# Performance work log

Measured on AMD Instinct MI355X. Metric: run time of the kernel, lower is better.

## Reference

```python
import jax, jax.numpy as jnp
import numpy as np
import math

N, E = 20000, 200000
MUL = 128            # multiplicity of the 0e and 1o channels
D = MUL + 3 * MUL    # 512 = node feature dim
EDGE_ATTR = 32
HID = 32             # invariant_neurons
LOG2 = math.log(2.0)


def ssp(x):
    # ShiftedSoftPlus
    return jax.nn.softplus(x) - LOG2


def split_irreps(x):
    # x: [?, 512] -> (l=0 part [?, MUL], l=1 part [?, MUL, 3])
    return x[:, :MUL], x[:, MUL:].reshape(x.shape[0], MUL, 3)


def merge_irreps(x0, x1):
    return jnp.concatenate([x0, x1.reshape(x1.shape[0], MUL * 3)], axis=-1)


def irrep_linear(x, W0, b0, W1):
    # e3nn o3.Linear: per-irrep channel mixing; bias only on l=0
    x0, x1 = split_irreps(x)
    y0 = x0 @ W0 + b0
    y1 = jnp.einsum('nuc,uv->nvc', x1, W1)
    return merge_irreps(y0, y1)


def setup_inputs() -> dict:
    key = jax.random.key(0)
    ks = iter(jax.random.split(key, 32))

    def randn(shape, scale=1.0):
        return (scale * jax.random.normal(next(ks), shape)).astype(jnp.float32)

    inp = {
        'x': randn((N, D)),
        'edge_sh': randn((E, 4)),
        'edge_attr': jax.random.uniform(next(ks), (E, EDGE_ATTR), dtype=jnp.float32),
        'edge_index': jax.random.randint(next(ks), (2, E), 0, N, dtype=jnp.int32),
        # linear_node_pre
        'W_pre0': randn((MUL, MUL), MUL ** -0.5), 'b_pre0': jnp.zeros((MUL,), jnp.float32),
        'W_pre1': randn((MUL, MUL), MUL ** -0.5),
        # linear_node
        'W_nd0': randn((MUL, MUL), MUL ** -0.5), 'b_nd0': jnp.zeros((MUL,), jnp.float32),
        'W_nd1': randn((MUL, MUL), MUL ** -0.5),
        # NormGate fc: Linear(2*MUL,2*MUL)+SiLU+Linear(2*MUL,2*MUL)
        'W_g1': randn((2 * MUL, 2 * MUL), (2 * MUL) ** -0.5), 'b_g1': jnp.zeros((2 * MUL,), jnp.float32),
        'W_g2': randn((2 * MUL, 2 * MUL), (2 * MUL) ** -0.5), 'b_g2': jnp.zeros((2 * MUL,), jnp.float32),
        # fc_node: FullyConnectedNet([32, 32, 4*MUL], ssp) -- no biases
        'W_f1': randn((EDGE_ATTR, HID), EDGE_ATTR ** -0.5),
        'W_f2': randn((HID, 4 * MUL), HID ** -0.5),
        # layer_l0: FullyConnectedNet([3*MUL, 32, 4*MUL], ssp)
        'W_s1': randn((3 * MUL, HID), (3 * MUL) ** -0.5),
        'W_s2': randn((HID, 4 * MUL), HID ** -0.5),
        # linear_out
        'W_o0': randn((MUL, MUL), MUL ** -0.5), 'b_o0': jnp.zeros((MUL,), jnp.float32),
        'W_o1': randn((MUL, MUL), MUL ** -0.5),
    }
    return inp


def reference(x, edge_sh, edge_attr, edge_index,
              W_pre0, b_pre0, W_pre1, W_nd0, b_nd0, W_nd1,
              W_g1, b_g1, W_g2, b_g2, W_f1, W_f2, W_s1, W_s2,
              W_o0, b_o0, W_o1):
    edge_dst, edge_src = edge_index[0], edge_index[1]
    old_x = x

    # ---- s0 edge invariants: linear_node_pre + InnerProduct (uuu, /dim)
    pre = irrep_linear(x, W_pre0, b_pre0, W_pre1)
    p0, p1 = split_irreps(pre)
    pd0 = p0[edge_dst]
    ip1 = jnp.einsum('eum,eum->eu', p1[edge_dst], p1[edge_src]) / 3.0   # l=1 inner product [E, MUL]
    s0 = jnp.concatenate([pd0, pd0, ip1], axis=-1)                      # [E, 3*MUL]

    # ---- NormGate then linear_node on node features
    x0, x1 = split_irreps(x)
    n1 = jnp.sqrt(jnp.sum(x1 * x1, axis=-1) / 3.0)                      # per-irrep norm [N, MUL]
    g = jax.nn.silu(jnp.concatenate([x0, n1], -1) @ W_g1 + b_g1) @ W_g2 + b_g2
    xg = merge_irreps(g[:, :MUL], x1 * g[:, MUL:, None])
    x = irrep_linear(xg, W_nd0, b_nd0, W_nd1)
    self_x = x

    # ---- per-edge tensor-product weights (fc_node(edge_attr) * layer_l0(s0))
    w = (ssp(edge_attr @ W_f1) @ W_f2) * (ssp(s0 @ W_s1) @ W_s2)        # [E, 4*MUL]
    w1, w2, w3, w4 = jnp.split(w, 4, axis=-1)

    # ---- gather + equivariant tensor product with edge spherical harmonics (uvu paths)
    x0e, x1e = split_irreps(x[edge_src])
    sh0, sh1 = edge_sh[:, 0], edge_sh[:, 1:4]
    # paths: 0e*0e->0e, 1o*1o->0e (dot), 0e*1o->1o, 1o*0e->1o
    out0 = w1 * x0e * sh0[:, None] + w4 * (jnp.einsum('eum,em->eu', x1e, sh1) / jnp.sqrt(3.0))
    out1 = (w2[:, :, None] * x0e[:, :, None] * sh1[:, None, :]
            + w3[:, :, None] * x1e * sh0[:, None, None])
    edge_feat = merge_irreps(out0, out1)                                # [E, D]

    # ---- scatter messages back to destination nodes
    out = jax.ops.segment_sum(edge_feat, edge_dst, num_segments=old_x.shape[0])
    out = out + self_x                                                  # irrep_in == irrep_out skip
    out = irrep_linear(out, W_o0, b_o0, W_o1)
    return out + old_x                                                  # ConvNetLayer resnet
```

## Files before the change

### kernel.cpp

```cpp
#include <hip/hip_runtime.h>
#include <hip/hip_fp16.h>
#include <math.h>

#define NN 20000
#define EE 200000

__device__ __forceinline__ float sspf(float x){
    float sp = (x > 20.f) ? x : log1pf(expf(x));
    return sp - 0.69314718056f;
}

__device__ __forceinline__ void fma8(float* acc, const float* base, float w){
    const float4 a = ((const float4*)base)[0];
    const float4 b = ((const float4*)base)[1];
    acc[0]+=a.x*w; acc[1]+=a.y*w; acc[2]+=a.z*w; acc[3]+=a.w*w;
    acc[4]+=b.x*w; acc[5]+=b.y*w; acc[6]+=b.z*w; acc[7]+=b.w*w;
}

__global__ __launch_bounds__(256) void k_pre(
    const float* __restrict__ x, const float* __restrict__ Wp0,
    const float* __restrict__ bp0, const float* __restrict__ Wp1,
    const float* __restrict__ Ws1,
    float* __restrict__ p1, float* __restrict__ sdst)
{
    __shared__ float xl[512][8];
    __shared__ float p0l[8][128];
    const int tid = threadIdx.x;
    const int n0 = blockIdx.x * 8;

    for (int it = 0; it < 4; ++it){
        int idx = tid + 256*it;
        int node = idx >> 7, o4 = idx & 127;
        float4 v = ((const float4*)(x + (size_t)(n0+node)*512))[o4];
        xl[o4*4+0][node]=v.x; xl[o4*4+1][node]=v.y;
        xl[o4*4+2][node]=v.z; xl[o4*4+3][node]=v.w;
    }
    __syncthreads();

    const int j = tid;
    float acc1[8] = {0,0,0,0,0,0,0,0};
    float acc2[8] = {0,0,0,0,0,0,0,0};
    const int o2 = j + 128;
    const int v2 = o2/3, m2 = o2%3;

    if (j < 128){
        for (int u = 0; u < 128; ++u){
            float w1 = Wp0[u*128 + j];
            float w2 = Wp1[u*128 + v2];
            fma8(acc1, &xl[u][0], w1);
            fma8(acc2, &xl[128 + u*3 + m2][0], w2);
        }
        float b = bp0[j];
        #pragma unroll
        for (int n = 0; n < 8; ++n) p0l[n][j] = acc1[n] + b;
    } else {
        const int o1 = j - 128, v1 = o1/3, m1 = o1%3;
        for (int u = 0; u < 128; ++u){
            float w1 = Wp1[u*128 + v1];
            float w2 = Wp1[u*128 + v2];
            fma8(acc1, &xl[128 + u*3 + m1][0], w1);
            fma8(acc2, &xl[128 + u*3 + m2][0], w2);
        }
        #pragma unroll
        for (int n = 0; n < 8; ++n) p1[(size_t)(n0+n)*384 + (j-128)] = acc1[n];
    }
    #pragma unroll
    for (int n = 0; n < 8; ++n) p1[(size_t)(n0+n)*384 + o2] = acc2[n];
    __syncthreads();

    {
        int n = tid >> 5, h = tid & 31;
        float s = 0.f;
        for (int u = 0; u < 128; ++u){
            float wc = Ws1[u*32 + h] + Ws1[(128+u)*32 + h];
            s += p0l[n][u] * wc;
        }
        sdst[(size_t)(n0+n)*32 + h] = s;
    }
}

__global__ __launch_bounds__(256) void k_gate_nd(
    const float* __restrict__ x,
    const float* __restrict__ Wg1, const float* __restrict__ bg1,
    const float* __restrict__ Wg2, const float* __restrict__ bg2,
    const float* __restrict__ Wnd0, const float* __restrict__ bnd0,
    const float* __restrict__ Wnd1,
    float* __restrict__ self_x)
{
    __shared__ float xl[512][8];
    __shared__ float tl[256][8];
    __shared__ float hl[256][8];
    const int tid = threadIdx.x;
    const int n0 = blockIdx.x * 8;

    for (int it = 0; it < 4; ++it){
        int idx = tid + 256*it;
        int node = idx >> 7, o4 = idx & 127;
        float4 v = ((const float4*)(x + (size_t)(n0+node)*512))[o4];
        xl[o4*4+0][node]=v.x; xl[o4*4+1][node]=v.y;
        xl[o4*4+2][node]=v.z; xl[o4*4+3][node]=v.w;
    }
    __syncthreads();

    {
        int jj = tid;
        if (jj < 128){
            #pragma unroll
            for (int n = 0; n < 8; ++n) tl[jj][n] = xl[jj][n];
        } else {
            int u = jj - 128;
            #pragma unroll
            for (int n = 0; n < 8; ++n){
                float a = xl[128+u*3][n], b = xl[128+u*3+1][n], c = xl[128+u*3+2][n];
                tl[jj][n] = sqrtf((a*a + b*b + c*c) * (1.f/3.f));
            }
        }
    }
    __syncthreads();

    {
        float acc[8] = {0,0,0,0,0,0,0,0};
        for (int k = 0; k < 256; ++k){
            float w = Wg1[k*256 + tid];
            fma8(acc, &tl[k][0], w);
        }
        float b = bg1[tid];
        #pragma unroll
        for (int n = 0; n < 8; ++n){
            float v = acc[n] + b;
            hl[tid][n] = v / (1.f + expf(-v));
        }
    }
    __syncthreads();

    {
        float acc[8] = {0,0,0,0,0,0,0,0};
        for (int k = 0; k < 256; ++k){
            float w = Wg2[k*256 + tid];
            fma8(acc, &hl[k][0], w);
        }
        float b = bg2[tid];
        #pragma unroll
        for (int n = 0; n < 8; ++n) tl[tid][n] = acc[n] + b;
    }
    __syncthreads();

    {
        int jj = tid;
        if (jj < 128){
            #pragma unroll
            for (int n = 0; n < 8; ++n) xl[jj][n] = tl[jj][n];
        } else {
            int u = jj - 128;
            #pragma unroll
            for (int n = 0; n < 8; ++n){
                float g1 = tl[128+u][n];
                xl[128+u*3  ][n] *= g1;
                xl[128+u*3+1][n] *= g1;
                xl[128+u*3+2][n] *= g1;
            }
        }
    }
    __syncthreads();

    const int j = tid;
    float acc1[8] = {0,0,0,0,0,0,0,0};
    float acc2[8] = {0,0,0,0,0,0,0,0};
    const int o2 = j + 128;
    const int v2 = o2/3, m2 = o2%3;
    if (j < 128){
        for (int u = 0; u < 128; ++u){
            float w1 = Wnd0[u*128 + j];
            float w2 = Wnd1[u*128 + v2];
            fma8(acc1, &xl[u][0], w1);
            fma8(acc2, &xl[128 + u*3 + m2][0], w2);
        }
        float b = bnd0[j];
        #pragma unroll
        for (int n = 0; n < 8; ++n) self_x[(size_t)(n0+n)*512 + j] = acc1[n] + b;
    } else {
        const int o1 = j - 128, v1 = o1/3, m1 = o1%3;
        for (int u = 0; u < 128; ++u){
            float w1 = Wnd1[u*128 + v1];
            float w2 = Wnd1[u*128 + v2];
            fma8(acc1, &xl[128 + u*3 + m1][0], w1);
            fma8(acc2, &xl[128 + u*3 + m2][0], w2);
        }
        #pragma unroll
        for (int n = 0; n < 8; ++n) self_x[(size_t)(n0+n)*512 + j] = acc1[n];
    }
    #pragma unroll
    for (int n = 0; n < 8; ++n) self_x[(size_t)(n0+n)*512 + j + 256] = acc2[n];
}

__global__ __launch_bounds__(256) void k_count(
    const int* __restrict__ eidx, int* __restrict__ cnt)
{
    int e = blockIdx.x * 256 + threadIdx.x;
    if (e < EE){
        int d = eidx[e];
        if (d >= 0 && d < NN) atomicAdd(&cnt[d], 1);
    }
}

__global__ __launch_bounds__(256) void k_scan(
    const int* __restrict__ cnt, int* __restrict__ rowptr, int* __restrict__ cur)
{
    __shared__ int part[256];
    const int t = threadIdx.x;
    const int CHUNK = 79;
    const int base = t * CHUNK;
    int s = 0;
    for (int i = 0; i < CHUNK; ++i){
        int idx = base + i;
        if (idx < NN) s += cnt[idx];
    }
    part[t] = s;
    __syncthreads();
    for (int off = 1; off < 256; off <<= 1){
        int v = (t >= off) ? part[t-off] : 0;
        __syncthreads();
        part[t] += v;
        __syncthreads();
    }
    int run = (t == 0) ? 0 : part[t-1];
    for (int i = 0; i < CHUNK; ++i){
        int idx = base + i;
        if (idx < NN){
            rowptr[idx] = run;
            cur[idx]    = run;
            run += cnt[idx];
        }
    }
    if (t == 255) rowptr[NN] = run;
}

__global__ __launch_bounds__(256) void k_fill(
    const int* __restrict__ eidx, int* __restrict__ cur, int2* __restrict__ ebuf,
    int* __restrict__ dstbuf)
{
    int e = blockIdx.x * 256 + threadIdx.x;
    if (e < EE){
        int dst = eidx[e];
        int src = eidx[EE + e];
        if (dst >= 0 && dst < NN){
            int pos = atomicAdd(&cur[dst], 1);
            if (pos >= 0 && pos < EE){
                ebuf[pos] = make_int2(e, src);
                dstbuf[pos] = dst;
            }
        }
    }
}

__global__ __launch_bounds__(256, 4) void k_edge_pre(
    const float* __restrict__ p1g, const float* __restrict__ sdst,
    const float* __restrict__ ea,
    const int2* __restrict__ ebuf, const int* __restrict__ dstbuf,
    const float* __restrict__ Wf1, const float* __restrict__ Ws1,
    float* __restrict__ fbuf, float* __restrict__ sbuf)
{
    __shared__ float ipw[4][128];
    const int tid  = threadIdx.x;
    const int wv   = tid >> 6, lane = tid & 63;
    const long e   = (long)blockIdx.x * 4 + wv;

    int2 pe = ebuf[e];
    if (!(pe.x >= 0 && pe.x < EE)) pe.x = 0;
    if (!(pe.y >= 0 && pe.y < NN)) pe.y = 0;
    int dst = dstbuf[e];
    if (!(dst >= 0 && dst < NN)) dst = 0;

    const float* pd = p1g + (size_t)dst*384 + lane*6;
    const float* ps = p1g + (size_t)pe.y*384 + lane*6;
    const float2 d01 = *(const float2*)(pd);
    const float2 d23 = *(const float2*)(pd+2);
    const float2 d45 = *(const float2*)(pd+4);
    const float2 s01 = *(const float2*)(ps);
    const float2 s23 = *(const float2*)(ps+2);
    const float2 s45 = *(const float2*)(ps+4);
    const float ipa = (d01.x*s01.x + d01.y*s01.y + d23.x*s23.x) * (1.f/3.f);
    const float ipb = (d23.y*s23.y + d45.x*s45.x + d45.y*s45.y) * (1.f/3.f);
    *(float2*)&ipw[wv][lane*2] = make_float2(ipa, ipb);

    const int h = lane & 31;
    const float sdv = sdst[(size_t)dst*32 + h];

    __syncthreads();

    const int uh = (lane >> 5) * 64;
    float sA = 0.f, sB = 0.f;
    #pragma unroll 8
    for (int uu = 0; uu < 64; uu += 2){
        sA += ipw[wv][uh+uu]   * Ws1[(256+uh+uu)*32 + h];
        sB += ipw[wv][uh+uu+1] * Ws1[(257+uh+uu)*32 + h];
    }
    float s = sA + sB;
    s += __shfl_xor(s, 32);

    const int kh = (lane >> 5) * 16;
    const float* ear = ea + (size_t)pe.x*32 + kh;
    float f = 0.f;
    #pragma unroll 8
    for (int kk = 0; kk < 16; ++kk)
        f += ear[kk] * Wf1[(kh+kk)*32 + h];
    f += __shfl_xor(f, 32);

    if (lane < 32){
        sbuf[e*32 + h] = sspf(s + sdv);
        fbuf[e*32 + h] = sspf(f);
    }
}

__global__ __launch_bounds__(256) void k_edge_one(
    const float* __restrict__ fbuf, const float* __restrict__ sbuf,
    const float* __restrict__ self_x, const float* __restrict__ esh,
    const int2* __restrict__ ebuf, const int* __restrict__ dstbuf,
    const float* __restrict__ Wf2, const float* __restrict__ Ws2,
    float* __restrict__ out)
{
    __shared__ float fbl[64][32];
    __shared__ float sbl[64][32];
    __shared__ float shl[64][4];
    __shared__ float sxl[4][128];
    __shared__ int   srcl[64], dl[64];

    const int tid = threadIdx.x;
    const int wv  = tid >> 6;
    const int ln  = tid & 63;
    const int c   = tid >> 1;
    const int h   = tid & 1;
    const long e0 = (long)blockIdx.x * 64;
    const float IS3 = 0.57735026919f;

    float wfA[32], wfB[32], wsA[32], wsB[32];
    {
        const int qA = 2*h*128 + c, qB = (2*h+1)*128 + c;
        #pragma unroll
        for (int k = 0; k < 32; ++k){
            wfA[k] = Wf2[(size_t)k*512 + qA];
            wfB[k] = Wf2[(size_t)k*512 + qB];
            wsA[k] = Ws2[(size_t)k*512 + qA];
            wsB[k] = Ws2[(size_t)k*512 + qB];
        }
    }

    if (tid < 64){
        int2 pe = ebuf[e0 + tid];
        if (!(pe.x >= 0 && pe.x < EE)) pe.x = 0;
        if (!(pe.y >= 0 && pe.y < NN)) pe.y = 0;
        int d = dstbuf[e0 + tid];
        if (!(d >= 0 && d < NN)) d = 0;
        srcl[tid] = pe.y; dl[tid] = d;
        ((float4*)shl)[tid] = ((const float4*)esh)[pe.x];
    }
    {
        const float4* fsrc = (const float4*)(fbuf + (size_t)e0*32);
        const float4* ssrc = (const float4*)(sbuf + (size_t)e0*32);
        ((float4*)fbl)[tid]       = fsrc[tid];
        ((float4*)fbl)[tid + 256] = fsrc[tid + 256];
        ((float4*)sbl)[tid]       = ssrc[tid];
        ((float4*)sbl)[tid + 256] = ssrc[tid + 256];
    }
    __syncthreads();

    const int dprev = (blockIdx.x == 0)    ? -1 : dstbuf[e0 - 1];
    const int dnext = (e0 + 64 < EE)       ? dstbuf[e0 + 64] : -1;

    const int goff = (ln < 16) ? (32*wv + 2*ln) : (128 + 96*wv + 2*(ln-16));
    const int loff = (ln < 16) ? (2*ln)         : (32 + 2*(ln-16));
    const int ci   = c & 31;

    float2 rA = *(const float2*)(self_x + (size_t)srcl[0]*512 + goff);
    float2 rB = *(const float2*)(self_x + (size_t)srcl[1]*512 + goff);
    float2 rC = *(const float2*)(self_x + (size_t)srcl[2]*512 + goff);
    *(float2*)&sxl[wv][loff] = rA;
    rA = rB; rB = rC;

    float a0 = 0.f, a1 = 0.f;
    int sstart = 0;

    for (int e = 0; e < 64; ++e){
        if (e < 61)
            rC = *(const float2*)(self_x + (size_t)srcl[e+3]*512 + goff);

        const float x0c = sxl[wv][ci];
        const float v0  = sxl[wv][32 + 3*ci];
        const float v1  = sxl[wv][32 + 3*ci + 1];
        const float v2  = sxl[wv][32 + 3*ci + 2];

        float FA = 0.f, FB = 0.f, SA = 0.f, SB = 0.f;
        #pragma unroll
        for (int k4 = 0; k4 < 8; ++k4){
            float4 fb4 = *(const float4*)&fbl[e][k4*4];
            float4 sb4 = *(const float4*)&sbl[e][k4*4];
            FA += fb4.x*wfA[k4*4+0]; FB += fb4.x*wfB[k4*4+0];
            SA += sb4.x*wsA[k4*4+0]; SB += sb4.x*wsB[k4*4+0];
            FA += fb4.y*wfA[k4*4+1]; FB += fb4.y*wfB[k4*4+1];
            SA += sb4.y*wsA[k4*4+1]; SB += sb4.y*wsB[k4*4+1];
            FA += fb4.z*wfA[k4*4+2]; FB += fb4.z*wfB[k4*4+2];
            SA += sb4.z*wsA[k4*4+2]; SB += sb4.z*wsB[k4*4+2];
            FA += fb4.w*wfA[k4*4+3]; FB += fb4.w*wfB[k4*4+3];
            SA += sb4.w*wsA[k4*4+3]; SB += sb4.w*wsB[k4*4+3];
        }
        const float wA = FA*SA, wB = FB*SB;
        const float oA = __shfl_xor(wA, 1);
        const float oB = __shfl_xor(wB, 1);
        const float w1 = h ? oA : wA;
        const float w2 = h ? oB : wB;
        const float w3 = h ? wA : oA;
        const float w4 = h ? wB : oB;

        const float4 sh = *(const float4*)&shl[e][0];
        const int dste = dl[e];

        const float dot = v0*sh.y + v1*sh.z + v2*sh.w;
        const float caw = h ? w2 : w1;
        const float cf  = h ? sh.z : sh.x;
        const float cbw = h ? w3 : w4*IS3;
        const float cg  = h ? v1*sh.x : dot;
        a0 += caw*x0c*cf + cbw*cg;
        const float shm = h ? sh.w : sh.y;
        const float vm  = h ? v2 : v0;
        a1 += w2*x0c*shm + w3*vm*sh.x;

        if (e == 63 || dl[e+1] != dste){
            const bool openL = (sstart == 0) && (dprev == dste);
            const bool openR = (e == 63) && (dnext == dste);
            float* orow = out + (size_t)dste*512;
            const int pos0 = h ? (128 + 3*c + 1) : c;
            const int pos1 = h ? (128 + 3*c + 2) : (128 + 3*c);
            if (openL || openR){
                atomicAdd(orow + pos0, a0);
                atomicAdd(orow + pos1, a1);
            } else {
                orow[pos0] = a0;
                orow[pos1] = a1;
            }
            a0 = 0.f; a1 = 0.f; sstart = e + 1;
        }

        if (e < 63){
            *(float2*)&sxl[wv][loff] = rA;
            rA = rB; rB = rC;
        }
    }
}

__global__ __launch_bounds__(256) void k_post(
    const float* __restrict__ self_x, const float* __restrict__ x,
    const float* __restrict__ Wo0, const float* __restrict__ bo0,
    const float* __restrict__ Wo1,
    float* __restrict__ out)
{
    __shared__ float tl[512][8];
    const int tid = threadIdx.x;
    const int n0 = blockIdx.x * 8;

    for (int it = 0; it < 4; ++it){
        int idx = tid + 256*it;
        int node = idx >> 7, o4 = idx & 127;
        float4 a = ((const float4*)(out    + (size_t)(n0+node)*512))[o4];
        float4 b = ((const float4*)(self_x + (size_t)(n0+node)*512))[o4];
        tl[o4*4+0][node]=a.x+b.x; tl[o4*4+1][node]=a.y+b.y;
        tl[o4*4+2][node]=a.z+b.z; tl[o4*4+3][node]=a.w+b.w;
    }
    __syncthreads();

    const int j = tid;
    float acc1[8] = {0,0,0,0,0,0,0,0};
    float acc2[8] = {0,0,0,0,0,0,0,0};
    const int o2 = j + 128;
    const int v2 = o2/3, m2 = o2%3;
    if (j < 128){
        for (int u = 0; u < 128; ++u){
            float w1 = Wo0[u*128 + j];
            float w2 = Wo1[u*128 + v2];
            fma8(acc1, &tl[u][0], w1);
            fma8(acc2, &tl[128 + u*3 + m2][0], w2);
        }
        float b = bo0[j];
        #pragma unroll
        for (int n = 0; n < 8; ++n)
            out[(size_t)(n0+n)*512 + j] = acc1[n] + b + x[(size_t)(n0+n)*512 + j];
    } else {
        const int o1 = j - 128, v1 = o1/3, m1 = o1%3;
        for (int u = 0; u < 128; ++u){
            float w1 = Wo1[u*128 + v1];
            float w2 = Wo1[u*128 + v2];
            fma8(acc1, &tl[128 + u*3 + m1][0], w1);
            fma8(acc2, &tl[128 + u*3 + m2][0], w2);
        }
        #pragma unroll
        for (int n = 0; n < 8; ++n)
            out[(size_t)(n0+n)*512 + j] = acc1[n] + x[(size_t)(n0+n)*512 + j];
    }
    #pragma unroll
    for (int n = 0; n < 8; ++n)
        out[(size_t)(n0+n)*512 + j + 256] = acc2[n] + x[(size_t)(n0+n)*512 + j + 256];
}

extern "C" void kernel_launch(void* const* d_in, const int* in_sizes, int n_in,
                              void* d_out, int out_size, void* d_ws, size_t ws_size,
                              hipStream_t stream)
{
    const float* x    = (const float*)d_in[0];
    const float* esh  = (const float*)d_in[1];
    const float* ea   = (const float*)d_in[2];
    const int*   eidx = (const int*)  d_in[3];
    const float* Wp0  = (const float*)d_in[4];
    const float* bp0  = (const float*)d_in[5];
    const float* Wp1  = (const float*)d_in[6];
    const float* Wnd0 = (const float*)d_in[7];
    const float* bnd0 = (const float*)d_in[8];
    const float* Wnd1 = (const float*)d_in[9];
    const float* Wg1  = (const float*)d_in[10];
    const float* bg1  = (const float*)d_in[11];
    const float* Wg2  = (const float*)d_in[12];
    const float* bg2  = (const float*)d_in[13];
    const float* Wf1  = (const float*)d_in[14];
    const float* Wf2  = (const float*)d_in[15];
    const float* Ws1  = (const float*)d_in[16];
    const float* Ws2  = (const float*)d_in[17];
    const float* Wo0  = (const float*)d_in[18];
    const float* bo0  = (const float*)d_in[19];
    const float* Wo1  = (const float*)d_in[20];

    float* out  = (float*)d_out;
    float* ws   = (float*)d_ws;
    float* p1   = ws;
    float* sdst = p1   + (size_t)NN*384;
    float* sfx  = sdst + (size_t)NN*32;
    float* fbuf = sfx  + (size_t)NN*512;
    float* sbuf = fbuf + (size_t)EE*32;

    int*  dcnt  = (int*)d_out;
    int*  dcur  = dcnt + NN;
    int*  drow  = dcur + NN;
    int2* debuf = (int2*)(drow + NN + 4);
    int*  ddst  = (int*)(debuf + EE);

    hipMemsetAsync(dcnt, 0, (size_t)NN*sizeof(int), stream);
    k_count <<<(EE+255)/256, 256, 0, stream>>>(eidx, dcnt);
    k_scan  <<<1, 256, 0, stream>>>(dcnt, drow, dcur);
    k_fill  <<<(EE+255)/256, 256, 0, stream>>>(eidx, dcur, debuf, ddst);

    k_pre     <<<NN/8, 256, 0, stream>>>(x, Wp0, bp0, Wp1, Ws1, p1, sdst);
    k_gate_nd <<<NN/8, 256, 0, stream>>>(x, Wg1, bg1, Wg2, bg2, Wnd0, bnd0, Wnd1, sfx);
    k_edge_pre<<<EE/4, 256, 0, stream>>>(p1, sdst, ea, debuf, ddst, Wf1, Ws1,
                                         fbuf, sbuf);

    int2* ebuf2   = (int2*)ws;
    int*  dstbuf2 = (int*)ws + (size_t)2*EE;
    hipMemcpyAsync(ws, debuf, (size_t)3*EE*sizeof(int),
                   hipMemcpyDeviceToDevice, stream);
    hipMemsetAsync(out, 0, (size_t)NN*512*sizeof(float), stream);

    k_edge_one<<<EE/64, 256, 0, stream>>>(fbuf, sbuf, sfx, esh, ebuf2, dstbuf2,
                                          Wf2, Ws2, out);

    k_post    <<<NN/8, 256, 0, stream>>>(sfx, x, Wo0, bo0, Wo1, out);
}
```

Before: 952.8 us.

## Transpose edge MLP weights and read per-edge hidden rows directly from global

```diff
diff --git a/kernel.cpp b/kernel.cpp
--- a/kernel.cpp
+++ b/kernel.cpp
@@ -253,6 +253,16 @@
     }
 }
 
+__global__ __launch_bounds__(256) void k_wt(
+    const float* __restrict__ Wf2, const float* __restrict__ Ws2,
+    float* __restrict__ Wtf, float* __restrict__ Wts)
+{
+    int idx = blockIdx.x*256 + threadIdx.x;
+    int q = idx >> 5, k = idx & 31;
+    Wtf[idx] = Wf2[(size_t)k*512 + q];
+    Wts[idx] = Ws2[(size_t)k*512 + q];
+}
+
 __global__ __launch_bounds__(256, 4) void k_edge_pre(
     const float* __restrict__ p1g, const float* __restrict__ sdst,
     const float* __restrict__ ea,
@@ -312,15 +322,13 @@
     }
 }
 
-__global__ __launch_bounds__(256) void k_edge_one(
+__global__ __launch_bounds__(256, 3) void k_edge_one(
     const float* __restrict__ fbuf, const float* __restrict__ sbuf,
     const float* __restrict__ self_x, const float* __restrict__ esh,
     const int2* __restrict__ ebuf, const int* __restrict__ dstbuf,
-    const float* __restrict__ Wf2, const float* __restrict__ Ws2,
+    const float* __restrict__ Wtf, const float* __restrict__ Wts,
     float* __restrict__ out)
 {
-    __shared__ float fbl[64][32];
-    __shared__ float sbl[64][32];
     __shared__ float shl[64][4];
     __shared__ float sxl[4][128];
     __shared__ int   srcl[64], dl[64];
@@ -333,15 +341,17 @@
     const long e0 = (long)blockIdx.x * 64;
     const float IS3 = 0.57735026919f;
 
-    float wfA[32], wfB[32], wsA[32], wsB[32];
+    float4 wfA[8], wfB[8], wsA[8], wsB[8];
     {
         const int qA = 2*h*128 + c, qB = (2*h+1)*128 + c;
-        #pragma unroll
-        for (int k = 0; k < 32; ++k){
-            wfA[k] = Wf2[(size_t)k*512 + qA];
-            wfB[k] = Wf2[(size_t)k*512 + qB];
-            wsA[k] = Ws2[(size_t)k*512 + qA];
-            wsB[k] = Ws2[(size_t)k*512 + qB];
+        const float4* pfA = (const float4*)(Wtf + (size_t)qA*32);
+        const float4* pfB = (const float4*)(Wtf + (size_t)qB*32);
+        const float4* psA = (const float4*)(Wts + (size_t)qA*32);
+        const float4* psB = (const float4*)(Wts + (size_t)qB*32);
+        #pragma unroll
+        for (int k4 = 0; k4 < 8; ++k4){
+            wfA[k4] = pfA[k4]; wfB[k4] = pfB[k4];
+            wsA[k4] = psA[k4]; wsB[k4] = psB[k4];
         }
     }
 
@@ -354,14 +364,6 @@
         srcl[tid] = pe.y; dl[tid] = d;
         ((float4*)shl)[tid] = ((const float4*)esh)[pe.x];
     }
-    {
-        const float4* fsrc = (const float4*)(fbuf + (size_t)e0*32);
-        const float4* ssrc = (const float4*)(sbuf + (size_t)e0*32);
-        ((float4*)fbl)[tid]       = fsrc[tid];
-        ((float4*)fbl)[tid + 256] = fsrc[tid + 256];
-        ((float4*)sbl)[tid]       = ssrc[tid];
-        ((float4*)sbl)[tid + 256] = ssrc[tid + 256];
-    }
     __syncthreads();
 
     const int dprev = (blockIdx.x == 0)    ? -1 : dstbuf[e0 - 1];
@@ -389,19 +391,21 @@
         const float v1  = sxl[wv][32 + 3*ci + 1];
         const float v2  = sxl[wv][32 + 3*ci + 2];
 
+        const float4* fbp = (const float4*)(fbuf + (size_t)(e0 + e)*32);
+        const float4* sbp = (const float4*)(sbuf + (size_t)(e0 + e)*32);
         float FA = 0.f, FB = 0.f, SA = 0.f, SB = 0.f;
         #pragma unroll
         for (int k4 = 0; k4 < 8; ++k4){
-            float4 fb4 = *(const float4*)&fbl[e][k4*4];
-            float4 sb4 = *(const float4*)&sbl[e][k4*4];
-            FA += fb4.x*wfA[k4*4+0]; FB += fb4.x*wfB[k4*4+0];
-            SA += sb4.x*wsA[k4*4+0]; SB += sb4.x*wsB[k4*4+0];
-            FA += fb4.y*wfA[k4*4+1]; FB += fb4.y*wfB[k4*4+1];
-            SA += sb4.y*wsA[k4*4+1]; SB += sb4.y*wsB[k4*4+1];
-            FA += fb4.z*wfA[k4*4+2]; FB += fb4.z*wfB[k4*4+2];
-            SA += sb4.z*wsA[k4*4+2]; SB += sb4.z*wsB[k4*4+2];
-            FA += fb4.w*wfA[k4*4+3]; FB += fb4.w*wfB[k4*4+3];
-            SA += sb4.w*wsA[k4*4+3]; SB += sb4.w*wsB[k4*4+3];
+            const float4 fb4 = fbp[k4];
+            const float4 sb4 = sbp[k4];
+            FA += fb4.x*wfA[k4].x; FA += fb4.y*wfA[k4].y;
+            FA += fb4.z*wfA[k4].z; FA += fb4.w*wfA[k4].w;
+            FB += fb4.x*wfB[k4].x; FB += fb4.y*wfB[k4].y;
+            FB += fb4.z*wfB[k4].z; FB += fb4.w*wfB[k4].w;
+            SA += sb4.x*wsA[k4].x; SA += sb4.y*wsA[k4].y;
+            SA += sb4.z*wsA[k4].z; SA += sb4.w*wsA[k4].w;
+            SB += sb4.x*wsB[k4].x; SB += sb4.y*wsB[k4].y;
+            SB += sb4.z*wsB[k4].z; SB += sb4.w*wsB[k4].w;
         }
         const float wA = FA*SA, wB = FB*SB;
         const float oA = __shfl_xor(wA, 1);
@@ -550,14 +554,17 @@
     k_edge_pre<<<EE/4, 256, 0, stream>>>(p1, sdst, ea, debuf, ddst, Wf1, Ws1,
                                          fbuf, sbuf);
 
-    int2* ebuf2   = (int2*)ws;
-    int*  dstbuf2 = (int*)ws + (size_t)2*EE;
+    int2*  ebuf2   = (int2*)ws;
+    int*   dstbuf2 = (int*)ws + (size_t)2*EE;
+    float* wtf     = ws + (size_t)3*EE;
+    float* wts     = wtf + 512*32;
+    k_wt<<<64, 256, 0, stream>>>(Wf2, Ws2, wtf, wts);
     hipMemcpyAsync(ws, debuf, (size_t)3*EE*sizeof(int),
                    hipMemcpyDeviceToDevice, stream);
     hipMemsetAsync(out, 0, (size_t)NN*512*sizeof(float), stream);
 
     k_edge_one<<<EE/64, 256, 0, stream>>>(fbuf, sbuf, sfx, esh, ebuf2, dstbuf2,
-                                          Wf2, Ws2, out);
+                                          wtf, wts, out);
 
     k_post    <<<NN/8, 256, 0, stream>>>(sfx, x, Wo0, bo0, Wo1, out);
 }
```

New measurement: 1.416 ms. 1.49x slower.
